# Kernel optimization log

Measured on AMD Instinct MI355X. Metric: run time of the kernel, lower is better.

## Reference

```python
import jax, jax.numpy as jnp
import numpy as np

NUM_BOXES = 16384
NUM_CLASS = 3
CODE_SIZE = 7
NMS_PRE = 1024
NMS_POST = 512
NMS_THRESH = 0.8
EPS = 1e-8


def _cross(a, b):
    return a[..., 0] * b[..., 1] - a[..., 1] * b[..., 0]


def _bev_corners(b5):
    # b5: (..., 5) = (cx, cy, dx, dy, ry) -> corners (..., 4, 2)
    c, s = jnp.cos(b5[..., 4]), jnp.sin(b5[..., 4])
    off = jnp.array([[0.5, 0.5], [-0.5, 0.5], [-0.5, -0.5], [0.5, -0.5]], dtype=b5.dtype)
    lx = b5[..., 2:3] * off[:, 0]  # (..., 4)
    ly = b5[..., 3:4] * off[:, 1]
    cx = b5[..., 0:1] + lx * c[..., None] - ly * s[..., None]
    cy = b5[..., 1:2] + lx * s[..., None] + ly * c[..., None]
    return jnp.stack([cx, cy], axis=-1)


def _points_in_box(p, b5):
    # p: (..., K, 2), b5: (..., 5) -> (..., K) bool (point inside rotated rect)
    c, s = jnp.cos(b5[..., 4:5]), jnp.sin(b5[..., 4:5])
    rel = p - b5[..., None, 0:2]
    qx = rel[..., 0] * c + rel[..., 1] * s
    qy = -rel[..., 0] * s + rel[..., 1] * c
    return (jnp.abs(qx) <= b5[..., 2:3] * 0.5 + 1e-5) & (jnp.abs(qy) <= b5[..., 3:4] * 0.5 + 1e-5)


def _pairwise_bev_iou(b5):
    # b5: (N, 5) -> (N, N) rotated BEV IoU (matches iou3d nms_gpu's BEV IoU)
    a = b5[:, None, :]
    b = b5[None, :, :]
    ca = _bev_corners(a)  # (N,1,4,2)
    cb = _bev_corners(b)  # (1,N,4,2)
    # edge-edge segment intersections: (N,N,4,4)
    a0, da = ca, jnp.roll(ca, -1, axis=-2) - ca
    b0, db = cb, jnp.roll(cb, -1, axis=-2) - cb
    A0, DA = a0[..., :, None, :], da[..., :, None, :]
    B0, DB = b0[..., None, :, :], db[..., None, :, :]
    den = _cross(DA, DB)
    d = B0 - A0
    den_s = jnp.where(jnp.abs(den) > EPS, den, 1.0)
    t = _cross(d, DB) / den_s
    u = _cross(d, DA) / den_s
    ok = (jnp.abs(den) > EPS) & (t >= 0) & (t <= 1) & (u >= 0) & (u <= 1)
    p_ee = A0 + t[..., None] * DA  # (N,N,4,4,2)
    shp = p_ee.shape[:-3]
    p_ee = p_ee.reshape(shp + (16, 2))
    ok = ok.reshape(shp + (16,))
    in_b = _points_in_box(ca, b)  # corners of A inside B: (N,N,4)
    in_a = _points_in_box(cb, a)  # corners of B inside A: (N,N,4)
    pts = jnp.concatenate([p_ee,
                           jnp.broadcast_to(ca, shp + (4, 2)),
                           jnp.broadcast_to(cb, shp + (4, 2))], axis=-2)  # (N,N,24,2)
    msk = jnp.concatenate([ok, in_b, in_a], axis=-1)  # (N,N,24)
    # order candidate vertices by angle around centroid (intersection is convex)
    cnt = jnp.maximum(msk.sum(-1, keepdims=True), 1)
    ctr = (pts * msk[..., None]).sum(-2, keepdims=True) / cnt[..., None]  # (N,N,1,2)
    ang = jnp.arctan2(pts[..., 1] - ctr[..., 1], pts[..., 0] - ctr[..., 0])
    ang = jnp.where(msk, ang, 1e9)  # invalid points sorted to the end
    order = jnp.argsort(ang, axis=-1)
    pts_s = jnp.take_along_axis(pts, order[..., None], axis=-2)
    msk_s = jnp.take_along_axis(msk, order, axis=-1)
    first = pts_s[..., 0:1, :]
    poly = jnp.where(msk_s[..., None], pts_s, first)  # pad with first vertex (zero shoelace contribution)
    inter = 0.5 * jnp.abs(_cross(poly, jnp.roll(poly, -1, axis=-2)).sum(-1))
    area_a = a[..., 2] * a[..., 3]
    area_b = b[..., 2] * b[..., 3]
    return inter / jnp.maximum(area_a + area_b - inter, 1e-6)


def _greedy_nms(iou, thresh):
    n = iou.shape[0]
    idx = jnp.arange(n)

    def body(i, supp):
        alive = jnp.logical_not(supp[i])
        return supp | (alive & (iou[i] > thresh) & (idx > i))

    supp = jax.lax.fori_loop(0, n, body, jnp.zeros((n,), dtype=bool))
    return ~supp


def _select_one(box_preds, cls_preds):
    # box_preds: (M, 7), cls_preds: (M, C) -> padded selected indices + validity
    scores = jnp.max(cls_preds, axis=1)
    _, top_idx = jax.lax.top_k(scores, NMS_PRE)  # score-descending, like torch.topk
    bev = box_preds[top_idx][:, jnp.array([0, 1, 3, 4, 6])]  # (cx,cy,dx,dy,ry)
    iou = _pairwise_bev_iou(bev)
    keep = _greedy_nms(iou, NMS_THRESH)
    pri = jnp.where(keep, jnp.arange(NMS_PRE), 2 * NMS_PRE)
    pos = jnp.sort(pri)[:NMS_POST]  # kept positions in score order
    valid = pos < NMS_PRE
    sel = top_idx[jnp.minimum(pos, NMS_PRE - 1)]
    return sel, valid


def setup_inputs() -> dict:
    key = jax.random.key(0)
    k1, k2, k3, k4, k5 = jax.random.split(key, 5)
    B = 2
    xy = jax.random.uniform(k1, (B, NUM_BOXES, 2), minval=-50.0, maxval=50.0)
    z = jax.random.uniform(k2, (B, NUM_BOXES, 1), minval=-2.0, maxval=1.0)
    dims = jax.random.uniform(k3, (B, NUM_BOXES, 3), minval=1.0, maxval=5.0)
    ry = jax.random.uniform(k4, (B, NUM_BOXES, 1), minval=-np.pi, maxval=np.pi)
    batch_box_preds = jnp.concatenate([xy, z, dims, ry], axis=-1).astype(jnp.float32)
    batch_cls_preds = (jax.random.normal(k5, (B, NUM_BOXES, NUM_CLASS)) * 3.0).astype(jnp.float32)
    return {"batch_box_preds": batch_box_preds, "batch_cls_preds": batch_cls_preds}


def reference(batch_box_preds, batch_cls_preds):
    # RoIHeadTemplate.proposal_layer: per-sample max-score, class-agnostic NMS,
    # scatter into zero-padded (B, NMS_POST, ...) tensors.
    sel, valid = jax.vmap(_select_one)(batch_box_preds, batch_cls_preds)  # (B, NMS_POST)
    rois = jnp.take_along_axis(batch_box_preds, sel[..., None], axis=1)
    logits = jnp.take_along_axis(batch_cls_preds, sel[..., None], axis=1)
    labels = jnp.argmax(logits, axis=-1)
    scores = jnp.max(logits, axis=-1)
    v = valid[..., None]
    rois = jnp.where(v, rois, 0.0)
    logits = jnp.where(v, logits, 0.0)
    scores = jnp.where(valid, scores, 0.0)
    roi_labels = jnp.where(valid, labels, 0) + 1  # padded slots end up as 1, same as torch (zeros + 1)
    return rois, scores, roi_labels, logits
```

## Files before the change

kernel.cpp:

```cpp
#include <hip/hip_runtime.h>
#include <hip/hip_bf16.h>
#include <math.h>

#define NBOX   16384
#define NPRE   1024
#define NPOST  512
#define NMS_TH 0.8f
#define DEN_EPS 1e-8f
#define NCAND  2048
#define NBUCK  8192
#define SEGCAP 16384
#define CANDL  2048

typedef unsigned long long ull;

__device__ __forceinline__ unsigned mono_f32(float a) {
  unsigned u = __float_as_uint(a);
  return (u & 0x80000000u) ? ~u : (u | 0x80000000u);
}

__global__ __launch_bounds__(256) void k_sel(
    const float* __restrict__ cls, ull* __restrict__ cand,
    unsigned* __restrict__ candCnt, unsigned* __restrict__ done) {
  __shared__ unsigned hist[NBUCK];
  __shared__ unsigned smallu[8];
  __shared__ unsigned thrT, cntL;
  const int b = blockIdx.x >> 3, s = blockIdx.x & 7;
  const int t = threadIdx.x;
  const int lane = t & 63, wv = t >> 6;
  const float* cb = cls + (size_t)b * NBOX * 3;

  if (blockIdx.x == 0 && t < 64) done[t] = 0u;
#pragma unroll
  for (int k = 0; k < NBUCK / 256; ++k) hist[t + k * 256] = 0u;
  if (t == 0) cntL = 0u;
  __syncthreads();

  for (int k = 0; k < 64; ++k) {
    int i = k * 256 + t;
    float sc = fmaxf(cb[i * 3], fmaxf(cb[i * 3 + 1], cb[i * 3 + 2]));
    atomicAdd(&hist[mono_f32(sc) >> 19], 1u);
  }
  __syncthreads();

  unsigned csum = 0;
#pragma unroll 8
  for (int k = 0; k < 32; ++k) csum += hist[t * 32 + k];
  unsigned v = csum;
#pragma unroll
  for (int off = 1; off < 64; off <<= 1) {
    unsigned o = __shfl_down((int)v, off, 64);
    if (lane + off < 64) v += o;
  }
  if (lane == 0) smallu[wv] = v;
  __syncthreads();
  unsigned shi = 0;
  for (int w2 = wv + 1; w2 < 4; ++w2) shi += smallu[w2];
  unsigned incl = v + shi;
  unsigned safter = incl - csum;
  if (safter < NPRE && incl >= NPRE) {
    unsigned c = safter;
    for (int k = 31; k >= 0; --k) {
      c += hist[t * 32 + k];
      if (c >= NPRE) { thrT = (unsigned)(t * 32 + k); break; }
    }
  }
  __syncthreads();
  unsigned T = thrT;

  ull* seg = cand + ((size_t)b * 8 + s) * 2048;
  for (int k = s * 8; k < s * 8 + 8; ++k) {
    int i = k * 256 + t;
    float sc = fmaxf(cb[i * 3], fmaxf(cb[i * 3 + 1], cb[i * 3 + 2]));
    unsigned u = mono_f32(sc);
    bool cnd = (u >> 19) >= T;
    ull bal = __ballot(cnd);
    if (bal) {
      unsigned base = 0;
      if (lane == 0) base = atomicAdd(&cntL, (unsigned)__popcll(bal));
      base = (unsigned)__shfl((int)base, 0, 64);
      if (cnd) {
        unsigned pos = base + (unsigned)__popcll(bal & ((1ull << lane) - 1ull));
        seg[pos] = (((ull)u) << 14) | (ull)(16383 - i);
      }
    }
  }
  __syncthreads();
  if (t == 0) candCnt[b * 8 + s] = cntL;
}

__global__ __launch_bounds__(256) void k_rank(
    const float* __restrict__ box, const ull* __restrict__ cand,
    const unsigned* __restrict__ candCnt,
    int* __restrict__ topi, float* __restrict__ binfo, float4* __restrict__ pinfoG) {
  __shared__ ull candL[NCAND];
  __shared__ unsigned offs[9];
  const int b = blockIdx.x >> 3, g = blockIdx.x & 7;
  const int t = threadIdx.x;

  if (t == 0) {
    unsigned o = 0;
    for (int s = 0; s < 8; ++s) {
      offs[s] = o;
      unsigned c = candCnt[b * 8 + s];
      o += (c < 2048u) ? c : 2048u;
    }
    offs[8] = o;
  }
  __syncthreads();
  unsigned C = offs[8]; if (C > NCAND) C = NCAND;
  for (int s = 0; s < 8; ++s) {
    unsigned base = offs[s], cnt = offs[s + 1] - offs[s];
    const ull* seg = cand + ((size_t)b * 8 + s) * 2048;
    for (unsigned e = (unsigned)t; e < cnt; e += 256) {
      unsigned dst = base + e;
      if (dst < NCAND) candL[dst] = seg[e];
    }
  }
  if (t < 2 && C + t < NCAND) candL[C + t] = 0ull;
  __syncthreads();

  int j = g * 256 + t;
  ull my = ((unsigned)j < C) ? candL[j] : 0ull;
  int r = 0;
  int kmax = (int)((C + 1) >> 1);
  const ulonglong2* p2 = (const ulonglong2*)candL;
  for (int k = 0; k < kmax; ++k) {
    ulonglong2 kk = p2[k];
    r += (kk.x > my) ? 1 : 0;
    r += (kk.y > my) ? 1 : 0;
  }
  if ((unsigned)j >= C || r >= NPRE) return;
  int i = 16383 - (int)(my & 0x3FFFULL);
  topi[b * NPRE + r] = i;
  const float* bp = box + ((size_t)b * NBOX + i) * 7;
  float x = bp[0], y = bp[1], dx = bp[3], dy = bp[4], ry = bp[6];
  float c = cosf(ry), s = sinf(ry);
  float* o = binfo + ((size_t)b * NPRE + r) * 16;
  o[0] = x; o[1] = y; o[2] = dx; o[3] = dy; o[4] = c; o[5] = s;
  const float offx[4] = {0.5f, -0.5f, -0.5f, 0.5f};
  const float offy[4] = {0.5f, 0.5f, -0.5f, -0.5f};
#pragma unroll
  for (int k = 0; k < 4; ++k) {
    float lx = dx * offx[k], ly = dy * offy[k];
    o[6 + k]  = x + lx * c - ly * s;
    o[10 + k] = y + lx * s + ly * c;
  }
  float rad = 0.5f * sqrtf(dx * dx + dy * dy);
  float area = dx * dy;
  o[14] = rad; o[15] = area;
  pinfoG[(size_t)b * NPRE + r] = make_float4(x, y, rad, area);
}

__device__ bool iou_exact_gt(const float* __restrict__ Ab, const float* __restrict__ Bb) {
  float ax = Ab[0], ay = Ab[1], bx = Bb[0], by = Bb[1];
  float aA = Ab[15], aB = Bb[15];
  float acx[4], acy[4], bcx[4], bcy[4];
#pragma unroll
  for (int k = 0; k < 4; ++k) {
    acx[k] = Ab[6 + k]; acy[k] = Ab[10 + k];
    bcx[k] = Bb[6 + k]; bcy[k] = Bb[10 + k];
  }
  float px[24], py[24];
  bool act[24];
#pragma unroll
  for (int p = 0; p < 4; ++p) {
    float A0x = acx[p], A0y = acy[p];
    float DAx = acx[(p + 1) & 3] - A0x, DAy = acy[(p + 1) & 3] - A0y;
#pragma unroll
    for (int q = 0; q < 4; ++q) {
      float B0x = bcx[q], B0y = bcy[q];
      float DBx = bcx[(q + 1) & 3] - B0x, DBy = bcy[(q + 1) & 3] - B0y;
      float den = DAx * DBy - DAy * DBx;
      float dxx = B0x - A0x, dyy = B0y - A0y;
      bool dok = fabsf(den) > DEN_EPS;
      float dens = dok ? den : 1.0f;
      float t = (dxx * DBy - dyy * DBx) / dens;
      float u = (dxx * DAy - dyy * DAx) / dens;
      int k = p * 4 + q;
      px[k] = A0x + t * DAx;
      py[k] = A0y + t * DAy;
      act[k] = dok && t >= 0.f && t <= 1.f && u >= 0.f && u <= 1.f;
    }
  }
  float cA = Ab[4], sA = Ab[5], cB = Bb[4], sB = Bb[5];
#pragma unroll
  for (int k = 0; k < 4; ++k) {
    float rx = acx[k] - bx, ry = acy[k] - by;
    float qx =  rx * cB + ry * sB, qy = -rx * sB + ry * cB;
    px[16 + k] = acx[k]; py[16 + k] = acy[k];
    act[16 + k] = (fabsf(qx) <= Bb[2] * 0.5f + 1e-5f) && (fabsf(qy) <= Bb[3] * 0.5f + 1e-5f);
  }
#pragma unroll
  for (int k = 0; k < 4; ++k) {
    float rx = bcx[k] - ax, ry = bcy[k] - ay;
    float qx =  rx * cA + ry * sA, qy = -rx * sA + ry * cA;
    px[20 + k] = bcx[k]; py[20 + k] = bcy[k];
    act[20 + k] = (fabsf(qx) <= Ab[2] * 0.5f + 1e-5f) && (fabsf(qy) <= Ab[3] * 0.5f + 1e-5f);
  }
  int cnt = 0; float sx = 0.f, sy = 0.f;
#pragma unroll
  for (int k = 0; k < 24; ++k)
    if (act[k]) { cnt++; sx += px[k]; sy += py[k]; }
  float fc = (float)(cnt > 1 ? cnt : 1);
  float cx0 = sx / fc, cy0 = sy / fc;
  ull key[24];
#pragma unroll
  for (int k = 0; k < 24; ++k) {
    float ang = atan2f(py[k] - cy0, px[k] - cx0);
    key[k] = act[k] ? ((((ull)mono_f32(ang)) << 5) | (ull)k) : ~0ull;
  }
  ull kmin = ~0ull; float fx = 0.f, fy = 0.f;
#pragma unroll
  for (int k = 0; k < 24; ++k) {
    bool lt = key[k] < kmin;
    kmin = lt ? key[k] : kmin;
    fx = lt ? px[k] : fx;
    fy = lt ? py[k] : fy;
  }
  float ssum = 0.f;
#pragma unroll
  for (int k = 0; k < 24; ++k) {
    ull myk = key[k];
    ull best = ~0ull; float nx = fx, ny = fy;
#pragma unroll
    for (int j = 0; j < 24; ++j) {
      bool c = (key[j] > myk) && (key[j] < best);
      best = c ? key[j] : best;
      nx = c ? px[j] : nx;
      ny = c ? py[j] : ny;
    }
    float contrib = px[k] * ny - py[k] * nx;
    ssum += (myk != ~0ull) ? contrib : 0.f;
  }
  float inter = 0.5f * fabsf(ssum);
  float uni = aA + aB - inter;
  return inter / fmaxf(uni, 1e-6f) > NMS_TH;
}

__device__ __forceinline__ int popbelow(const unsigned* rowbm, int i) {
  int s = 0, w = i >> 5;
  for (int k = 0; k < w; ++k) s += __popc(rowbm[k]);
  s += __popc(rowbm[w] & ((1u << (i & 31)) - 1u));
  return s;
}

__global__ __launch_bounds__(512) void k_pairsfin(
    const float4* __restrict__ pinfoG, const float* __restrict__ binfo,
    const float* __restrict__ box, const float* __restrict__ cls,
    const int* __restrict__ topi,
    unsigned* __restrict__ hitseg, unsigned* __restrict__ hitcnt,
    unsigned* __restrict__ done, float* __restrict__ out, int B) {
  __shared__ float4 pin[NPRE];
  __shared__ unsigned candL[CANDL];
  __shared__ unsigned cntC, cntH;
  __shared__ int amLast;
  const int b = blockIdx.x >> 6, blk = blockIdx.x & 63;
  const int t = threadIdx.x;
  const int lane = t & 63, wv = t >> 6;
#pragma unroll
  for (int k = 0; k < 2; ++k) pin[k * 512 + t] = pinfoG[(size_t)b * NPRE + k * 512 + t];
  if (t == 0) { cntC = 0u; cntH = 0u; }
  __syncthreads();

  const float* bi = binfo + (size_t)b * NPRE * 16;
  unsigned sbase = ((unsigned)b * 64 + (unsigned)blk) * SEGCAP;
  for (int iter = 0; iter < 32; ++iter) {
    int task = iter * 8 + wv;
    int q = task >> 4, w = task & 15;
    int i = q * 64 + blk;
    if (w * 64 + 63 <= i) continue;
    int j = w * 64 + lane;
    float4 pi = pin[i];
    float4 pj = pin[j];
    bool cnd = false;
    if (j > i) {
      float ddx = pi.x - pj.x, ddy = pi.y - pj.y;
      float rr = pi.z + pj.z + 1e-3f;
      if (ddx * ddx + ddy * ddy <= rr * rr) {
        float mn = fminf(pi.w, pj.w), mx = fmaxf(pi.w, pj.w);
        if (mn > NMS_TH * mx) cnd = true;
      }
    }
    ull bal = __ballot(cnd);
    if (!bal) continue;
    unsigned base = 0;
    if (lane == 0) base = atomicAdd(&cntC, (unsigned)__popcll(bal));
    base = (unsigned)__shfl((int)base, 0, 64);
    if (cnd) {
      unsigned off = base + (unsigned)__popcll(bal & ((1ull << lane) - 1ull));
      unsigned pk = ((unsigned)i << 10) | (unsigned)j;
      if (off < CANDL) candL[off] = pk;
      else {
        if (iou_exact_gt(bi + (size_t)i * 16, bi + (size_t)j * 16)) {
          unsigned h = atomicAdd(&cntH, 1u);
          hitseg[sbase + h] = pk;
        }
      }
    }
  }
  __syncthreads();

  unsigned C = cntC; if (C > CANDL) C = CANDL;
  for (unsigned e = (unsigned)t; e < C; e += 512) {
    unsigned pk = candL[e];
    unsigned i = pk >> 10, j = pk & 1023u;
    if (iou_exact_gt(bi + (size_t)i * 16, bi + (size_t)j * 16)) {
      unsigned h = atomicAdd(&cntH, 1u);
      hitseg[sbase + h] = pk;
    }
  }
  __syncthreads();
  if (t == 0) {
    hitcnt[b * 64 + blk] = (cntH < (unsigned)SEGCAP) ? cntH : (unsigned)SEGCAP;
    __threadfence();
    unsigned old = atomicAdd(&done[b], 1u);
    amLast = (old == 63u) ? 1 : 0;
  }
  __syncthreads();
  if (!amLast) return;
  __threadfence();

  unsigned* maskL = (unsigned*)pin;
  unsigned* rlist = candL;
  __shared__ unsigned segoff[65];
  __shared__ unsigned scnt[64];
  __shared__ unsigned rowbm[32];
  __shared__ ull remv_sh[16];
  __shared__ unsigned smallu[8];
  __shared__ unsigned rn_sh;

  for (int k = t; k < 128 * 32; k += 512) maskL[k] = 0u;
  if (t < 32) rowbm[t] = 0u;
  if (t < 64) scnt[t] = hitcnt[b * 64 + t];
  __syncthreads();
  if (t == 0) {
    unsigned o = 0;
    for (int s = 0; s < 64; ++s) {
      segoff[s] = o;
      unsigned c = scnt[s];
      o += (c < (unsigned)SEGCAP) ? c : (unsigned)SEGCAP;
    }
    segoff[64] = o;
  }
  __syncthreads();
  unsigned H = segoff[64];

  for (unsigned e = (unsigned)t; e < H; e += 512) {
    int lo = 0, hi = 63;
    while (lo < hi) { int mid = (lo + hi + 1) >> 1; if (segoff[mid] <= e) lo = mid; else hi = mid - 1; }
    unsigned pk = hitseg[((size_t)(b * 64 + lo)) * SEGCAP + (e - segoff[lo])];
    atomicOr(&rowbm[(pk >> 10) >> 5], 1u << ((pk >> 10) & 31));
  }
  __syncthreads();
  for (int row = t; row < NPRE; row += 512) {
    if ((rowbm[row >> 5] >> (row & 31)) & 1u)
      rlist[popbelow(rowbm, row)] = (unsigned)row;
  }
  if (t == 0) {
    unsigned s = 0;
    for (int w = 0; w < 32; ++w) s += (unsigned)__popc(rowbm[w]);
    rn_sh = s;
  }
  __syncthreads();
  for (unsigned e = (unsigned)t; e < H; e += 512) {
    int lo = 0, hi = 63;
    while (lo < hi) { int mid = (lo + hi + 1) >> 1; if (segoff[mid] <= e) lo = mid; else hi = mid - 1; }
    unsigned pk = hitseg[((size_t)(b * 64 + lo)) * SEGCAP + (e - segoff[lo])];
    unsigned i = pk >> 10, j = pk & 1023u;
    int slot = popbelow(rowbm, (int)i);
    if (slot < 128) atomicOr(&maskL[slot * 32 + (j >> 5)], 1u << (j & 31));
  }
  __syncthreads();

  if (wv == 0) {
    ull remv = 0;
    unsigned rn = rn_sh;
    for (unsigned s = 0; s < rn; ++s) {
      unsigned row = rlist[s];
      ull m = 0;
      if (s < 128) {
        if (lane < 16)
          m = (ull)maskL[s * 32 + lane * 2] | ((ull)maskL[s * 32 + lane * 2 + 1] << 32);
      } else {
        for (unsigned e = 0; e < H; ++e) {
          int lo = 0, hi = 63;
          while (lo < hi) { int mid = (lo + hi + 1) >> 1; if (segoff[mid] <= e) lo = mid; else hi = mid - 1; }
          unsigned pk = hitseg[((size_t)(b * 64 + lo)) * SEGCAP + (e - segoff[lo])];
          if ((pk >> 10) == row) {
            unsigned j = pk & 1023u;
            if (lane == (int)(j >> 6)) m |= 1ull << (j & 63);
          }
        }
      }
      ull rw = __shfl(remv, (int)(row >> 6), 64);
      if (!((rw >> (row & 63)) & 1ULL)) remv |= m;
    }
    if (lane < 16) remv_sh[lane] = remv;
  }
  __syncthreads();

  int p0 = t * 2;
  ull rw = remv_sh[p0 >> 6];
  int a0 = ((rw >> (p0 & 63)) & 1ULL) ? 0 : 1;
  int a1 = ((rw >> ((p0 + 1) & 63)) & 1ULL) ? 0 : 1;
  int myc = a0 + a1;
  int v = myc;
#pragma unroll
  for (int off = 1; off < 64; off <<= 1) {
    int t2 = __shfl_up(v, off, 64);
    if (lane >= off) v += t2;
  }
  if (lane == 63) smallu[wv] = (unsigned)v;
  __syncthreads();
  int pre = 0;
  for (int w2 = 0; w2 < wv; ++w2) pre += (int)smallu[w2];
  int total = 0;
  for (int w2 = 0; w2 < 8; ++w2) total += (int)smallu[w2];
  int s = pre + v - myc;

  float* rois   = out;
  float* scores = out + (size_t)B * NPOST * 7;
  float* labels = scores + (size_t)B * NPOST;
  float* logits = labels + (size_t)B * NPOST;
  int aa[2] = {a0, a1};
#pragma unroll
  for (int k = 0; k < 2; ++k) {
    if (aa[k] && s < NPOST) {
      int orig = topi[b * NPRE + p0 + k];
      const float* bb = box + ((size_t)b * NBOX + orig) * 7;
      float* ro = rois + ((size_t)b * NPOST + s) * 7;
#pragma unroll
      for (int c2 = 0; c2 < 7; ++c2) ro[c2] = bb[c2];
      const float* cc = cls + ((size_t)b * NBOX + orig) * 3;
      float l0 = cc[0], l1 = cc[1], l2 = cc[2];
      float m = fmaxf(l0, fmaxf(l1, l2));
      int lab = (l0 == m) ? 0 : ((l1 == m) ? 1 : 2);
      scores[b * NPOST + s] = m;
      labels[b * NPOST + s] = (float)(lab + 1);
      float* lg = logits + ((size_t)b * NPOST + s) * 3;
      lg[0] = l0; lg[1] = l1; lg[2] = l2;
    }
    s += aa[k];
  }
  if (t < NPOST && t >= total) {
    float* ro = rois + ((size_t)b * NPOST + t) * 7;
#pragma unroll
    for (int c2 = 0; c2 < 7; ++c2) ro[c2] = 0.f;
    scores[b * NPOST + t] = 0.f;
    labels[b * NPOST + t] = 1.f;
    float* lg = logits + ((size_t)b * NPOST + t) * 3;
    lg[0] = 0.f; lg[1] = 0.f; lg[2] = 0.f;
  }
}

extern "C" void kernel_launch(void* const* d_in, const int* in_sizes, int n_in,
                              void* d_out, int out_size, void* d_ws, size_t ws_size,
                              hipStream_t stream) {
  const float* box = (const float*)d_in[0];
  const float* cls = (const float*)d_in[1];
  float* out = (float*)d_out;
  int B = in_sizes[0] / (NBOX * 7);

  char* w = (char*)d_ws;
  size_t off = 0;
  ull* cand        = (ull*)(w + off);      off += (size_t)B * 8 * 2048 * sizeof(ull);
  unsigned* candCt = (unsigned*)(w + off); off += (size_t)B * 8 * sizeof(unsigned);
  int* topi        = (int*)(w + off);      off += (size_t)B * NPRE * sizeof(int);
  unsigned* hitcnt = (unsigned*)(w + off); off += (size_t)B * 64 * sizeof(unsigned);
  unsigned* done   = (unsigned*)(w + off); off += 64 * sizeof(unsigned);
  off = (off + 63) & ~(size_t)63;
  float* binfo     = (float*)(w + off);    off += (size_t)B * NPRE * 16 * sizeof(float);
  float4* pinfoG   = (float4*)(w + off);   off += (size_t)B * NPRE * sizeof(float4);
  unsigned* hitseg = (unsigned*)(w + off); off += (size_t)B * 64 * SEGCAP * sizeof(unsigned);
  (void)off; (void)ws_size; (void)out_size; (void)n_in;

  hipLaunchKernelGGL(k_sel,      dim3(B * 8),  dim3(256), 0, stream, cls, cand, candCt, done);
  hipLaunchKernelGGL(k_rank,     dim3(B * 8),  dim3(256), 0, stream, box, cand, candCt, topi, binfo, pinfoG);
  hipLaunchKernelGGL(k_pairsfin, dim3(B * 64), dim3(512), 0, stream, pinfoG, binfo, box, cls, topi,
                     hitseg, hitcnt, done, out, B);
}
```

Measured before the change: 127.6 us.

## Fuse candidate selection and ranking into one block-per-batch kernel

Merges the histogram-threshold selection kernel and the rank kernel into one 512-thread kernel. Candidates are compacted straight into shared memory, so the global candidate buffer, the count array and one launch boundary go away. Each thread now ranks four candidates, which amortises the shared-memory scan over the candidate list. The grid stays at B*8 blocks while each block now handles a whole batch, so the eight blocks per batch repeat the same work and write identical results. That adds redundant compute and stores in exchange for dropping a launch.

```diff
diff --git a/kernel.cpp b/kernel.cpp
--- a/kernel.cpp
+++ b/kernel.cpp
@@ -19,33 +19,35 @@
   return (u & 0x80000000u) ? ~u : (u | 0x80000000u);
 }
 
-__global__ __launch_bounds__(256) void k_sel(
-    const float* __restrict__ cls, ull* __restrict__ cand,
-    unsigned* __restrict__ candCnt, unsigned* __restrict__ done) {
+__global__ __launch_bounds__(512) void k_selrank(
+    const float* __restrict__ box, const float* __restrict__ cls,
+    int* __restrict__ topi, float* __restrict__ binfo,
+    float4* __restrict__ pinfoG, unsigned* __restrict__ done) {
   __shared__ unsigned hist[NBUCK];
+  __shared__ ull candL[NCAND];
   __shared__ unsigned smallu[8];
   __shared__ unsigned thrT, cntL;
-  const int b = blockIdx.x >> 3, s = blockIdx.x & 7;
+  const int b = blockIdx.x >> 3;
   const int t = threadIdx.x;
   const int lane = t & 63, wv = t >> 6;
   const float* cb = cls + (size_t)b * NBOX * 3;
 
   if (blockIdx.x == 0 && t < 64) done[t] = 0u;
 #pragma unroll
-  for (int k = 0; k < NBUCK / 256; ++k) hist[t + k * 256] = 0u;
+  for (int k = 0; k < NBUCK / 512; ++k) hist[t + k * 512] = 0u;
   if (t == 0) cntL = 0u;
   __syncthreads();
 
-  for (int k = 0; k < 64; ++k) {
-    int i = k * 256 + t;
+  for (int k = 0; k < 32; ++k) {
+    int i = k * 512 + t;
     float sc = fmaxf(cb[i * 3], fmaxf(cb[i * 3 + 1], cb[i * 3 + 2]));
     atomicAdd(&hist[mono_f32(sc) >> 19], 1u);
   }
   __syncthreads();
 
   unsigned csum = 0;
-#pragma unroll 8
-  for (int k = 0; k < 32; ++k) csum += hist[t * 32 + k];
+#pragma unroll
+  for (int k = 0; k < 16; ++k) csum += hist[t * 16 + k];
   unsigned v = csum;
 #pragma unroll
   for (int off = 1; off < 64; off <<= 1) {
@@ -55,22 +57,21 @@
   if (lane == 0) smallu[wv] = v;
   __syncthreads();
   unsigned shi = 0;
-  for (int w2 = wv + 1; w2 < 4; ++w2) shi += smallu[w2];
+  for (int w2 = wv + 1; w2 < 8; ++w2) shi += smallu[w2];
   unsigned incl = v + shi;
   unsigned safter = incl - csum;
   if (safter < NPRE && incl >= NPRE) {
     unsigned c = safter;
-    for (int k = 31; k >= 0; --k) {
-      c += hist[t * 32 + k];
-      if (c >= NPRE) { thrT = (unsigned)(t * 32 + k); break; }
+    for (int k = 15; k >= 0; --k) {
+      c += hist[t * 16 + k];
+      if (c >= NPRE) { thrT = (unsigned)(t * 16 + k); break; }
     }
   }
   __syncthreads();
   unsigned T = thrT;
 
-  ull* seg = cand + ((size_t)b * 8 + s) * 2048;
-  for (int k = s * 8; k < s * 8 + 8; ++k) {
-    int i = k * 256 + t;
+  for (int k = 0; k < 32; ++k) {
+    int i = k * 512 + t;
     float sc = fmaxf(cb[i * 3], fmaxf(cb[i * 3 + 1], cb[i * 3 + 2]));
     unsigned u = mono_f32(sc);
     bool cnd = (u >> 19) >= T;
@@ -81,75 +82,59 @@
       base = (unsigned)__shfl((int)base, 0, 64);
       if (cnd) {
         unsigned pos = base + (unsigned)__popcll(bal & ((1ull << lane) - 1ull));
-        seg[pos] = (((ull)u) << 14) | (ull)(16383 - i);
+        if (pos < NCAND) candL[pos] = (((ull)u) << 14) | (ull)(16383 - i);
       }
     }
   }
   __syncthreads();
-  if (t == 0) candCnt[b * 8 + s] = cntL;
-}
-
-__global__ __launch_bounds__(256) void k_rank(
-    const float* __restrict__ box, const ull* __restrict__ cand,
-    const unsigned* __restrict__ candCnt,
-    int* __restrict__ topi, float* __restrict__ binfo, float4* __restrict__ pinfoG) {
-  __shared__ ull candL[NCAND];
-  __shared__ unsigned offs[9];
-  const int b = blockIdx.x >> 3, g = blockIdx.x & 7;
-  const int t = threadIdx.x;
-
-  if (t == 0) {
-    unsigned o = 0;
-    for (int s = 0; s < 8; ++s) {
-      offs[s] = o;
-      unsigned c = candCnt[b * 8 + s];
-      o += (c < 2048u) ? c : 2048u;
-    }
-    offs[8] = o;
-  }
-  __syncthreads();
-  unsigned C = offs[8]; if (C > NCAND) C = NCAND;
-  for (int s = 0; s < 8; ++s) {
-    unsigned base = offs[s], cnt = offs[s + 1] - offs[s];
-    const ull* seg = cand + ((size_t)b * 8 + s) * 2048;
-    for (unsigned e = (unsigned)t; e < cnt; e += 256) {
-      unsigned dst = base + e;
-      if (dst < NCAND) candL[dst] = seg[e];
-    }
-  }
+  unsigned C = cntL; if (C > NCAND) C = NCAND;
   if (t < 2 && C + t < NCAND) candL[C + t] = 0ull;
   __syncthreads();
 
-  int j = g * 256 + t;
-  ull my = ((unsigned)j < C) ? candL[j] : 0ull;
-  int r = 0;
+  ull my0 = ((unsigned)t          < C) ? candL[t]          : 0ull;
+  ull my1 = ((unsigned)t + 512u   < C) ? candL[t + 512]    : 0ull;
+  ull my2 = ((unsigned)t + 1024u  < C) ? candL[t + 1024]   : 0ull;
+  ull my3 = ((unsigned)t + 1536u  < C) ? candL[t + 1536]   : 0ull;
+  int r0 = 0, r1 = 0, r2 = 0, r3 = 0;
   int kmax = (int)((C + 1) >> 1);
   const ulonglong2* p2 = (const ulonglong2*)candL;
   for (int k = 0; k < kmax; ++k) {
     ulonglong2 kk = p2[k];
-    r += (kk.x > my) ? 1 : 0;
-    r += (kk.y > my) ? 1 : 0;
-  }
-  if ((unsigned)j >= C || r >= NPRE) return;
-  int i = 16383 - (int)(my & 0x3FFFULL);
-  topi[b * NPRE + r] = i;
-  const float* bp = box + ((size_t)b * NBOX + i) * 7;
-  float x = bp[0], y = bp[1], dx = bp[3], dy = bp[4], ry = bp[6];
-  float c = cosf(ry), s = sinf(ry);
-  float* o = binfo + ((size_t)b * NPRE + r) * 16;
-  o[0] = x; o[1] = y; o[2] = dx; o[3] = dy; o[4] = c; o[5] = s;
-  const float offx[4] = {0.5f, -0.5f, -0.5f, 0.5f};
-  const float offy[4] = {0.5f, 0.5f, -0.5f, -0.5f};
-#pragma unroll
-  for (int k = 0; k < 4; ++k) {
-    float lx = dx * offx[k], ly = dy * offy[k];
-    o[6 + k]  = x + lx * c - ly * s;
-    o[10 + k] = y + lx * s + ly * c;
-  }
-  float rad = 0.5f * sqrtf(dx * dx + dy * dy);
-  float area = dx * dy;
-  o[14] = rad; o[15] = area;
-  pinfoG[(size_t)b * NPRE + r] = make_float4(x, y, rad, area);
+    r0 += (kk.x > my0) ? 1 : 0; r0 += (kk.y > my0) ? 1 : 0;
+    r1 += (kk.x > my1) ? 1 : 0; r1 += (kk.y > my1) ? 1 : 0;
+    r2 += (kk.x > my2) ? 1 : 0; r2 += (kk.y > my2) ? 1 : 0;
+    r3 += (kk.x > my3) ? 1 : 0; r3 += (kk.y > my3) ? 1 : 0;
+  }
+
+  const float* boxb = box + (size_t)b * NBOX * 7;
+  ull myk[4] = {my0, my1, my2, my3};
+  int  rk[4] = {r0, r1, r2, r3};
+#pragma unroll
+  for (int sl = 0; sl < 4; ++sl) {
+    unsigned e = (unsigned)t + (unsigned)sl * 512u;
+    int r = rk[sl];
+    if (e < C && r < NPRE) {
+      int i = 16383 - (int)(myk[sl] & 0x3FFFULL);
+      topi[b * NPRE + r] = i;
+      const float* bp = boxb + (size_t)i * 7;
+      float x = bp[0], y = bp[1], dx = bp[3], dy = bp[4], ry = bp[6];
+      float c = cosf(ry), s = sinf(ry);
+      float* o = binfo + ((size_t)b * NPRE + r) * 16;
+      o[0] = x; o[1] = y; o[2] = dx; o[3] = dy; o[4] = c; o[5] = s;
+      const float offx[4] = {0.5f, -0.5f, -0.5f, 0.5f};
+      const float offy[4] = {0.5f, 0.5f, -0.5f, -0.5f};
+#pragma unroll
+      for (int k = 0; k < 4; ++k) {
+        float lx = dx * offx[k], ly = dy * offy[k];
+        o[6 + k]  = x + lx * c - ly * s;
+        o[10 + k] = y + lx * s + ly * c;
+      }
+      float rad = 0.5f * sqrtf(dx * dx + dy * dy);
+      float area = dx * dy;
+      o[14] = rad; o[15] = area;
+      pinfoG[(size_t)b * NPRE + r] = make_float4(x, y, rad, area);
+    }
+  }
 }
 
 __device__ bool iou_exact_gt(const float* __restrict__ Ab, const float* __restrict__ Bb) {
@@ -464,8 +449,6 @@
 
   char* w = (char*)d_ws;
   size_t off = 0;
-  ull* cand        = (ull*)(w + off);      off += (size_t)B * 8 * 2048 * sizeof(ull);
-  unsigned* candCt = (unsigned*)(w + off); off += (size_t)B * 8 * sizeof(unsigned);
   int* topi        = (int*)(w + off);      off += (size_t)B * NPRE * sizeof(int);
   unsigned* hitcnt = (unsigned*)(w + off); off += (size_t)B * 64 * sizeof(unsigned);
   unsigned* done   = (unsigned*)(w + off); off += 64 * sizeof(unsigned);
@@ -475,8 +458,7 @@
   unsigned* hitseg = (unsigned*)(w + off); off += (size_t)B * 64 * SEGCAP * sizeof(unsigned);
   (void)off; (void)ws_size; (void)out_size; (void)n_in;
 
-  hipLaunchKernelGGL(k_sel,      dim3(B * 8),  dim3(256), 0, stream, cls, cand, candCt, done);
-  hipLaunchKernelGGL(k_rank,     dim3(B * 8),  dim3(256), 0, stream, box, cand, candCt, topi, binfo, pinfoG);
+  hipLaunchKernelGGL(k_selrank,  dim3(B * 8),  dim3(512), 0, stream, box, cls, topi, binfo, pinfoG, done);
   hipLaunchKernelGGL(k_pairsfin, dim3(B * 64), dim3(512), 0, stream, pinfoG, binfo, box, cls, topi,
                      hitseg, hitcnt, done, out, B);
 }
```

New measurement: 147.5 us. 1.16x slower.
